# Kernel tuning notes

Measured on AMD Instinct MI355X. Metric: run time of the kernel, lower is better.

Reference implementation:

```python
import jax, jax.numpy as jnp
import numpy as np

B, T, C, H, W = 1, 8, 128, 64, 64
F = 64  # num_feat


def setup_inputs() -> dict:
    key = jax.random.key(0)
    ks = jax.random.split(key, 8)
    return {
        "input1": jax.random.normal(ks[0], (B, T, C, H, W), jnp.float32),
        "input2": jax.random.normal(ks[1], (B, T, C, H, W), jnp.float32),
        "W1": jax.random.normal(ks[2], (F, C), jnp.float32) * 0.05,
        "b1": jax.random.normal(ks[3], (F,), jnp.float32) * 0.05,
        "W2": jax.random.normal(ks[4], (F, C), jnp.float32) * 0.05,
        "b2": jax.random.normal(ks[5], (F,), jnp.float32) * 0.05,
        "W3": jax.random.normal(ks[6], (F, C), jnp.float32) * 0.05,
        "b3": jax.random.normal(ks[7], (F,), jnp.float32) * 0.05,
    }


def reference(input1, input2, W1, b1, W2, b2, W3, b3):
    # act == 0 (ReLU branch). Conv1d(kernel=1) == per-position linear projection.
    b, t, c, h, w = input1.shape
    n = h * w
    x1 = input1.reshape(b, t, c, n)  # matches transpose(1,2).reshape then frame slice
    x2 = input2.reshape(b, t, c, n)
    q = jnp.einsum('fc,btcn->btnf', W1, x1) + b1          # [B,T,N,F]
    k = jnp.einsum('fc,btcn->btnf', W2, x2) + b2          # [B,T,N,F]
    g = jnp.einsum('fc,btcn->btnf', W3, x1) + b3          # [B,T,N,F]
    scores = jax.nn.relu(jnp.einsum('btnf,btmf->btnm', q, k))  # [B,T,N,N]
    out = jnp.einsum('btnm,btmf->btnf', scores, g)        # [B,T,N,F]
    # view([B,H,W,F]).permute(0,3,1,2), stacked over T -> [B,T,F,H,W]
    return out.reshape(b, t, h, w, -1).transpose(0, 1, 4, 2, 3)
```

## Files before the change

kernel.cpp:

```cpp
#include <hip/hip_runtime.h>
#include <hip/hip_bf16.h>

constexpr int T = 8;
constexpr int C = 128;
constexpr int N = 4096;
constexpr int F = 64;

typedef __bf16 bf16x8 __attribute__((ext_vector_type(8)));
typedef __bf16 bf16x4 __attribute__((ext_vector_type(4)));
typedef float  f32x4  __attribute__((ext_vector_type(4)));

__global__ __launch_bounds__(256) void prep_w_kernel(
    const float* __restrict__ W1, const float* __restrict__ W2,
    const float* __restrict__ W3, __bf16* __restrict__ Wb)
{
    int i = blockIdx.x * 256 + threadIdx.x;
    const float* Ws[3] = {W1, W2, W3};
    int p = i >> 13, r = i & 8191;
    Wb[i] = (__bf16)Ws[p][r];
}

__global__ __launch_bounds__(256) void zero_out_kernel(float* __restrict__ out)
{
    int i = blockIdx.x * 256 + threadIdx.x;
    ((f32x4*)out)[i] = (f32x4){0.f, 0.f, 0.f, 0.f};
}

__global__ __launch_bounds__(256) void proj_kernel(
    const float* __restrict__ x1, const float* __restrict__ x2,
    const __bf16* __restrict__ Wb,
    const float* __restrict__ b1, const float* __restrict__ b2,
    const float* __restrict__ b3,
    __bf16* __restrict__ Qb, __bf16* __restrict__ Kb, __bf16* __restrict__ Gw)
{
    const int t  = blockIdx.x >> 6;
    const int nb = blockIdx.x & 63;
    const int n0 = nb * 64;

    constexpr int XS = C + 8;
    __shared__ __bf16 Xt1[64 * XS];
    __shared__ __bf16 Xt2[64 * XS];

    const int tid = threadIdx.x;
#pragma unroll
    for (int rep = 0; rep < 32; ++rep) {
        int idx = rep * 256 + tid;
        int c = idx >> 6, nl = idx & 63;
        size_t goff = ((size_t)t * C + c) * (size_t)N + n0 + nl;
        Xt1[nl * XS + c] = (__bf16)x1[goff];
        Xt2[nl * XS + c] = (__bf16)x2[goff];
    }
    __syncthreads();

    const int wave = tid >> 6, lane = tid & 63;
    const int quad = lane >> 4, l16 = lane & 15;

    bf16x8 a1[4], a2[4];
#pragma unroll
    for (int cc = 0; cc < 4; ++cc) {
        a1[cc] = *(const bf16x8*)&Xt1[(wave * 16 + l16) * XS + cc * 32 + quad * 8];
        a2[cc] = *(const bf16x8*)&Xt2[(wave * 16 + l16) * XS + cc * 32 + quad * 8];
    }

#pragma unroll
    for (int p = 0; p < 2; ++p) {
        const __bf16* W    = Wb + (size_t)p * F * C;
        const float*  bias = p ? b2 : b1;
        __bf16*       O    = p ? Kb : Qb;

        f32x4 acc[4];
#pragma unroll
        for (int ft = 0; ft < 4; ++ft) acc[ft] = (f32x4){0.f, 0.f, 0.f, 0.f};
#pragma unroll
        for (int cc = 0; cc < 4; ++cc) {
#pragma unroll
            for (int ft = 0; ft < 4; ++ft) {
                bf16x8 b = *(const bf16x8*)&W[(ft * 16 + l16) * C + cc * 32 + quad * 8];
                bf16x8 a = p ? a2[cc] : a1[cc];
                acc[ft] = __builtin_amdgcn_mfma_f32_16x16x32_bf16(a, b, acc[ft], 0, 0, 0);
            }
        }
#pragma unroll
        for (int ft = 0; ft < 4; ++ft) {
            int f = ft * 16 + l16;
            float bv = bias[f];
#pragma unroll
            for (int r = 0; r < 4; ++r) {
                int n = n0 + wave * 16 + quad * 4 + r;
                O[((size_t)t * N + n) * F + f] = (__bf16)(acc[ft][r] + bv);
            }
        }
    }

    {
        const __bf16* W3b = Wb + (size_t)2 * F * C;
        bf16x8 wa[4];
#pragma unroll
        for (int cc = 0; cc < 4; ++cc)
            wa[cc] = *(const bf16x8*)&W3b[(wave * 16 + l16) * C + cc * 32 + quad * 8];

        f32x4 acc[4];
#pragma unroll
        for (int nt = 0; nt < 4; ++nt) acc[nt] = (f32x4){0.f, 0.f, 0.f, 0.f};
#pragma unroll
        for (int cc = 0; cc < 4; ++cc) {
#pragma unroll
            for (int nt = 0; nt < 4; ++nt) {
                bf16x8 b = *(const bf16x8*)&Xt1[(nt * 16 + l16) * XS + cc * 32 + quad * 8];
                acc[nt] = __builtin_amdgcn_mfma_f32_16x16x32_bf16(wa[cc], b, acc[nt], 0, 0, 0);
            }
        }
#pragma unroll
        for (int nt = 0; nt < 4; ++nt) {
#pragma unroll
            for (int r = 0; r < 4; ++r) {
                int f = wave * 16 + quad * 4 + r;
                int n = n0 + nt * 16 + l16;
                Gw[((size_t)t * F + f) * (size_t)N + n] = (__bf16)(acc[nt][r] + b3[f]);
            }
        }
    }
}

constexpr int KSPLIT = 2;

__global__ __launch_bounds__(256) void attn_kernel(
    const __bf16* __restrict__ Qb, const __bf16* __restrict__ Kb,
    const __bf16* __restrict__ Gw, float* __restrict__ out)
{
    const int ks = blockIdx.x & (KSPLIT - 1);
    const int qb = (blockIdx.x / KSPLIT) & 31;
    const int t  = blockIdx.x / (KSPLIT * 32);
    const int q0 = qb * 128;

    constexpr int KS = 72;
    __shared__ __bf16 Kt[64 * KS];
    __shared__ __bf16 Gt[64 * KS];
    __shared__ __bf16 Sb[128 * KS];

    const int tid = threadIdx.x, wave = tid >> 6, lane = tid & 63;
    const int quad = lane >> 4, l16 = lane & 15;

    bf16x8 qf[2][2];
#pragma unroll
    for (int qg = 0; qg < 2; ++qg) {
        const __bf16* qrow = &Qb[((size_t)t * N + q0 + wave * 32 + qg * 16 + l16) * F];
        qf[qg][0] = *(const bf16x8*)&qrow[quad * 8];
        qf[qg][1] = *(const bf16x8*)&qrow[32 + quad * 8];
    }

    f32x4 oacc[4][2];
#pragma unroll
    for (int ft = 0; ft < 4; ++ft)
#pragma unroll
        for (int qg = 0; qg < 2; ++qg) oacc[ft][qg] = (f32x4){0.f, 0.f, 0.f, 0.f};

    const int kb_lo = ks * (N / 64 / KSPLIT);
    const int kb_hi = kb_lo + (N / 64 / KSPLIT);

    const int r8a = tid >> 3,          c8a = (tid & 7) * 8;
    const int r8b = (tid + 256) >> 3,  c8b = c8a;

    bf16x8 kv0, kv1, gv0, gv1;
    {
        const int k0 = kb_lo * 64;
        kv0 = *(const bf16x8*)&Kb[((size_t)t * N + k0 + r8a) * F + c8a];
        kv1 = *(const bf16x8*)&Kb[((size_t)t * N + k0 + r8b) * F + c8b];
        gv0 = *(const bf16x8*)&Gw[((size_t)t * F + r8a) * (size_t)N + k0 + c8a];
        gv1 = *(const bf16x8*)&Gw[((size_t)t * F + r8b) * (size_t)N + k0 + c8b];
    }

    for (int kb = kb_lo; kb < kb_hi; ++kb) {
        __syncthreads();
        *(bf16x8*)&Kt[r8a * KS + c8a] = kv0;
        *(bf16x8*)&Kt[r8b * KS + c8b] = kv1;
        *(bf16x8*)&Gt[r8a * KS + c8a] = gv0;
        *(bf16x8*)&Gt[r8b * KS + c8b] = gv1;
        __syncthreads();

        if (kb + 1 < kb_hi) {
            const int k0 = (kb + 1) * 64;
            kv0 = *(const bf16x8*)&Kb[((size_t)t * N + k0 + r8a) * F + c8a];
            kv1 = *(const bf16x8*)&Kb[((size_t)t * N + k0 + r8b) * F + c8b];
            gv0 = *(const bf16x8*)&Gw[((size_t)t * F + r8a) * (size_t)N + k0 + c8a];
            gv1 = *(const bf16x8*)&Gw[((size_t)t * F + r8b) * (size_t)N + k0 + c8b];
        }

#pragma unroll
        for (int nt = 0; nt < 4; ++nt) {
            bf16x8 k0f = *(const bf16x8*)&Kt[(nt * 16 + l16) * KS + quad * 8];
            bf16x8 k1f = *(const bf16x8*)&Kt[(nt * 16 + l16) * KS + 32 + quad * 8];
#pragma unroll
            for (int qg = 0; qg < 2; ++qg) {
                f32x4 s = (f32x4){0.f, 0.f, 0.f, 0.f};
                s = __builtin_amdgcn_mfma_f32_16x16x32_bf16(k0f, qf[qg][0], s, 0, 0, 0);
                s = __builtin_amdgcn_mfma_f32_16x16x32_bf16(k1f, qf[qg][1], s, 0, 0, 0);
                bf16x4 sp;
#pragma unroll
                for (int r = 0; r < 4; ++r) sp[r] = (__bf16)fmaxf(s[r], 0.f);
                *(bf16x4*)&Sb[(wave * 32 + qg * 16 + l16) * KS + nt * 16 + quad * 4] = sp;
            }
        }

        bf16x8 sf[2][2];
#pragma unroll
        for (int qg = 0; qg < 2; ++qg) {
            const __bf16* srow = &Sb[(wave * 32 + qg * 16 + l16) * KS];
            sf[qg][0] = *(const bf16x8*)&srow[quad * 8];
            sf[qg][1] = *(const bf16x8*)&srow[32 + quad * 8];
        }
#pragma unroll
        for (int ft = 0; ft < 4; ++ft) {
            bf16x8 g0 = *(const bf16x8*)&Gt[(ft * 16 + l16) * KS + quad * 8];
            bf16x8 g1 = *(const bf16x8*)&Gt[(ft * 16 + l16) * KS + 32 + quad * 8];
#pragma unroll
            for (int qg = 0; qg < 2; ++qg) {
                oacc[ft][qg] = __builtin_amdgcn_mfma_f32_16x16x32_bf16(g0, sf[qg][0], oacc[ft][qg], 0, 0, 0);
                oacc[ft][qg] = __builtin_amdgcn_mfma_f32_16x16x32_bf16(g1, sf[qg][1], oacc[ft][qg], 0, 0, 0);
            }
        }
    }

#pragma unroll
    for (int ft = 0; ft < 4; ++ft)
#pragma unroll
        for (int qg = 0; qg < 2; ++qg)
#pragma unroll
            for (int r = 0; r < 4; ++r) {
                int f = ft * 16 + quad * 4 + r;
                int q = q0 + wave * 32 + qg * 16 + l16;
                unsafeAtomicAdd(&out[((size_t)t * F + f) * (size_t)N + q], oacc[ft][qg][r]);
            }
}

extern "C" void kernel_launch(void* const* d_in, const int* in_sizes, int n_in,
                              void* d_out, int out_size, void* d_ws, size_t ws_size,
                              hipStream_t stream) {
    const float* x1 = (const float*)d_in[0];
    const float* x2 = (const float*)d_in[1];
    const float* W1 = (const float*)d_in[2];
    const float* b1 = (const float*)d_in[3];
    const float* W2 = (const float*)d_in[4];
    const float* b2 = (const float*)d_in[5];
    const float* W3 = (const float*)d_in[6];
    const float* b3 = (const float*)d_in[7];
    float* out = (float*)d_out;

    __bf16* Qb = (__bf16*)d_ws;
    __bf16* Kb = Qb + (size_t)T * N * F;
    __bf16* Gw = Kb + (size_t)T * N * F;
    __bf16* Wb = Gw + (size_t)T * N * F;

    prep_w_kernel<<<dim3(3 * F * C / 256), dim3(256), 0, stream>>>(W1, W2, W3, Wb);
    proj_kernel<<<dim3(T * (N / 64)), dim3(256), 0, stream>>>(
        x1, x2, Wb, b1, b2, b3, Qb, Kb, Gw);
    zero_out_kernel<<<dim3(T * F * N / 4 / 256), dim3(256), 0, stream>>>(out);
    attn_kernel<<<dim3(T * 32 * KSPLIT), dim3(256), 0, stream>>>(Qb, Kb, Gw, out);
}
```

Baseline: 162.3 us.

## Fuse weight prep and output zeroing into projection, enlarge attention query tile

Removes the separate weight-conversion and output-zeroing kernels. The projection kernel now zeroes its slice of the output, converts fp32 weights to bf16 on the fly, and loads x directly into MFMA fragments without an LDS transpose. The attention kernel now processes 256 queries per block (64 per wave) with KSPLIT raised to 4, which doubles K/G reuse per LDS tile while keeping the same grid size. The trade is higher register and LDS pressure, uncoalesced strided x loads, and redundant weight conversion in every block.

Measured after the change: 166.7 us. 1.03x slower.

```diff
diff --git a/kernel.cpp b/kernel.cpp
--- a/kernel.cpp
+++ b/kernel.cpp
@@ -10,150 +10,109 @@
 typedef __bf16 bf16x4 __attribute__((ext_vector_type(4)));
 typedef float  f32x4  __attribute__((ext_vector_type(4)));
 
-__global__ __launch_bounds__(256) void prep_w_kernel(
-    const float* __restrict__ W1, const float* __restrict__ W2,
-    const float* __restrict__ W3, __bf16* __restrict__ Wb)
-{
-    int i = blockIdx.x * 256 + threadIdx.x;
-    const float* Ws[3] = {W1, W2, W3};
-    int p = i >> 13, r = i & 8191;
-    Wb[i] = (__bf16)Ws[p][r];
-}
-
-__global__ __launch_bounds__(256) void zero_out_kernel(float* __restrict__ out)
-{
-    int i = blockIdx.x * 256 + threadIdx.x;
-    ((f32x4*)out)[i] = (f32x4){0.f, 0.f, 0.f, 0.f};
-}
-
 __global__ __launch_bounds__(256) void proj_kernel(
     const float* __restrict__ x1, const float* __restrict__ x2,
-    const __bf16* __restrict__ Wb,
-    const float* __restrict__ b1, const float* __restrict__ b2,
-    const float* __restrict__ b3,
-    __bf16* __restrict__ Qb, __bf16* __restrict__ Kb, __bf16* __restrict__ Gw)
+    const float* __restrict__ W1, const float* __restrict__ b1,
+    const float* __restrict__ W2, const float* __restrict__ b2,
+    const float* __restrict__ W3, const float* __restrict__ b3,
+    __bf16* __restrict__ Qb, __bf16* __restrict__ Kb, __bf16* __restrict__ Gw,
+    float* __restrict__ out)
 {
-    const int t  = blockIdx.x >> 6;
-    const int nb = blockIdx.x & 63;
-    const int n0 = nb * 64;
-
-    constexpr int XS = C + 8;
-    __shared__ __bf16 Xt1[64 * XS];
-    __shared__ __bf16 Xt2[64 * XS];
-
-    const int tid = threadIdx.x;
-#pragma unroll
-    for (int rep = 0; rep < 32; ++rep) {
-        int idx = rep * 256 + tid;
-        int c = idx >> 6, nl = idx & 63;
-        size_t goff = ((size_t)t * C + c) * (size_t)N + n0 + nl;
-        Xt1[nl * XS + c] = (__bf16)x1[goff];
-        Xt2[nl * XS + c] = (__bf16)x2[goff];
-    }
-    __syncthreads();
-
-    const int wave = tid >> 6, lane = tid & 63;
+    const int t   = blockIdx.x >> 6;
+    const int nb  = blockIdx.x & 63;
+    const int tid = threadIdx.x, wave = tid >> 6, lane = tid & 63;
     const int quad = lane >> 4, l16 = lane & 15;
-
-    bf16x8 a1[4], a2[4];
+    const int nw = nb * 64 + wave * 16;
+
+    {
+        f32x4* o4 = (f32x4*)out + (size_t)blockIdx.x * 1024;
+#pragma unroll
+        for (int i = 0; i < 4; ++i) o4[i * 256 + tid] = (f32x4){0.f, 0.f, 0.f, 0.f};
+    }
+
+    bf16x8 xf1[4], xf2[4];
 #pragma unroll
     for (int cc = 0; cc < 4; ++cc) {
-        a1[cc] = *(const bf16x8*)&Xt1[(wave * 16 + l16) * XS + cc * 32 + quad * 8];
-        a2[cc] = *(const bf16x8*)&Xt2[(wave * 16 + l16) * XS + cc * 32 + quad * 8];
-    }
-
-#pragma unroll
-    for (int p = 0; p < 2; ++p) {
-        const __bf16* W    = Wb + (size_t)p * F * C;
-        const float*  bias = p ? b2 : b1;
-        __bf16*       O    = p ? Kb : Qb;
-
-        f32x4 acc[4];
-#pragma unroll
-        for (int ft = 0; ft < 4; ++ft) acc[ft] = (f32x4){0.f, 0.f, 0.f, 0.f};
-#pragma unroll
-        for (int cc = 0; cc < 4; ++cc) {
-#pragma unroll
-            for (int ft = 0; ft < 4; ++ft) {
-                bf16x8 b = *(const bf16x8*)&W[(ft * 16 + l16) * C + cc * 32 + quad * 8];
-                bf16x8 a = p ? a2[cc] : a1[cc];
-                acc[ft] = __builtin_amdgcn_mfma_f32_16x16x32_bf16(a, b, acc[ft], 0, 0, 0);
-            }
-        }
-#pragma unroll
-        for (int ft = 0; ft < 4; ++ft) {
-            int f = ft * 16 + l16;
-            float bv = bias[f];
-#pragma unroll
-            for (int r = 0; r < 4; ++r) {
-                int n = n0 + wave * 16 + quad * 4 + r;
-                O[((size_t)t * N + n) * F + f] = (__bf16)(acc[ft][r] + bv);
-            }
-        }
-    }
-
-    {
-        const __bf16* W3b = Wb + (size_t)2 * F * C;
-        bf16x8 wa[4];
-#pragma unroll
-        for (int cc = 0; cc < 4; ++cc)
-            wa[cc] = *(const bf16x8*)&W3b[(wave * 16 + l16) * C + cc * 32 + quad * 8];
-
-        f32x4 acc[4];
-#pragma unroll
-        for (int nt = 0; nt < 4; ++nt) acc[nt] = (f32x4){0.f, 0.f, 0.f, 0.f};
-#pragma unroll
-        for (int cc = 0; cc < 4; ++cc) {
-#pragma unroll
-            for (int nt = 0; nt < 4; ++nt) {
-                bf16x8 b = *(const bf16x8*)&Xt1[(nt * 16 + l16) * XS + cc * 32 + quad * 8];
-                acc[nt] = __builtin_amdgcn_mfma_f32_16x16x32_bf16(wa[cc], b, acc[nt], 0, 0, 0);
-            }
-        }
-#pragma unroll
-        for (int nt = 0; nt < 4; ++nt) {
-#pragma unroll
-            for (int r = 0; r < 4; ++r) {
-                int f = wave * 16 + quad * 4 + r;
-                int n = n0 + nt * 16 + l16;
-                Gw[((size_t)t * F + f) * (size_t)N + n] = (__bf16)(acc[nt][r] + b3[f]);
+#pragma unroll
+        for (int j = 0; j < 8; ++j) {
+            size_t off = ((size_t)t * C + cc * 32 + quad * 8 + j) * (size_t)N + nw + l16;
+            xf1[cc][j] = (__bf16)x1[off];
+            xf2[cc][j] = (__bf16)x2[off];
+        }
+    }
+
+    const float* Ws[3] = {W1, W2, W3};
+    const float* bs[3] = {b1, b2, b3};
+
+#pragma unroll
+    for (int p = 0; p < 3; ++p) {
+        const float* W    = Ws[p];
+        const float* bias = bs[p];
+#pragma unroll
+        for (int fb = 0; fb < 4; ++fb) {
+            f32x4 acc = (f32x4){0.f, 0.f, 0.f, 0.f};
+#pragma unroll
+            for (int cc = 0; cc < 4; ++cc) {
+                const f32x4* wp = (const f32x4*)&W[(fb * 16 + l16) * C + cc * 32 + quad * 8];
+                f32x4 w0 = wp[0], w1 = wp[1];
+                bf16x8 wf;
+                wf[0] = (__bf16)w0[0]; wf[1] = (__bf16)w0[1];
+                wf[2] = (__bf16)w0[2]; wf[3] = (__bf16)w0[3];
+                wf[4] = (__bf16)w1[0]; wf[5] = (__bf16)w1[1];
+                wf[6] = (__bf16)w1[2]; wf[7] = (__bf16)w1[3];
+                bf16x8 xb = (p == 1) ? xf2[cc] : xf1[cc];
+                acc = __builtin_amdgcn_mfma_f32_16x16x32_bf16(wf, xb, acc, 0, 0, 0);
+            }
+            if (p < 2) {
+                __bf16* O = p ? Kb : Qb;
+                bf16x4 ov;
+#pragma unroll
+                for (int r = 0; r < 4; ++r)
+                    ov[r] = (__bf16)(acc[r] + bias[fb * 16 + quad * 4 + r]);
+                *(bf16x4*)&O[((size_t)t * N + nw + l16) * F + fb * 16 + quad * 4] = ov;
+            } else {
+#pragma unroll
+                for (int r = 0; r < 4; ++r) {
+                    int f = fb * 16 + quad * 4 + r;
+                    Gw[((size_t)t * F + f) * (size_t)N + nw + l16] = (__bf16)(acc[r] + bias[f]);
+                }
             }
         }
     }
 }
 
-constexpr int KSPLIT = 2;
+constexpr int KSPLIT = 4;
 
 __global__ __launch_bounds__(256) void attn_kernel(
     const __bf16* __restrict__ Qb, const __bf16* __restrict__ Kb,
     const __bf16* __restrict__ Gw, float* __restrict__ out)
 {
     const int ks = blockIdx.x & (KSPLIT - 1);
-    const int qb = (blockIdx.x / KSPLIT) & 31;
-    const int t  = blockIdx.x / (KSPLIT * 32);
-    const int q0 = qb * 128;
+    const int qb = (blockIdx.x / KSPLIT) & 15;
+    const int t  = blockIdx.x >> 6;
+    const int q0 = qb * 256;
 
     constexpr int KS = 72;
     __shared__ __bf16 Kt[64 * KS];
     __shared__ __bf16 Gt[64 * KS];
-    __shared__ __bf16 Sb[128 * KS];
+    __shared__ __bf16 Sb[256 * KS];
 
     const int tid = threadIdx.x, wave = tid >> 6, lane = tid & 63;
     const int quad = lane >> 4, l16 = lane & 15;
 
-    bf16x8 qf[2][2];
-#pragma unroll
-    for (int qg = 0; qg < 2; ++qg) {
-        const __bf16* qrow = &Qb[((size_t)t * N + q0 + wave * 32 + qg * 16 + l16) * F];
+    bf16x8 qf[4][2];
+#pragma unroll
+    for (int qg = 0; qg < 4; ++qg) {
+        const __bf16* qrow = &Qb[((size_t)t * N + q0 + wave * 64 + qg * 16 + l16) * F];
         qf[qg][0] = *(const bf16x8*)&qrow[quad * 8];
         qf[qg][1] = *(const bf16x8*)&qrow[32 + quad * 8];
     }
 
-    f32x4 oacc[4][2];
+    f32x4 oacc[4][4];
 #pragma unroll
     for (int ft = 0; ft < 4; ++ft)
 #pragma unroll
-        for (int qg = 0; qg < 2; ++qg) oacc[ft][qg] = (f32x4){0.f, 0.f, 0.f, 0.f};
+        for (int qg = 0; qg < 4; ++qg) oacc[ft][qg] = (f32x4){0.f, 0.f, 0.f, 0.f};
 
     const int kb_lo = ks * (N / 64 / KSPLIT);
     const int kb_hi = kb_lo + (N / 64 / KSPLIT);
@@ -191,21 +150,21 @@
             bf16x8 k0f = *(const bf16x8*)&Kt[(nt * 16 + l16) * KS + quad * 8];
             bf16x8 k1f = *(const bf16x8*)&Kt[(nt * 16 + l16) * KS + 32 + quad * 8];
 #pragma unroll
-            for (int qg = 0; qg < 2; ++qg) {
+            for (int qg = 0; qg < 4; ++qg) {
                 f32x4 s = (f32x4){0.f, 0.f, 0.f, 0.f};
                 s = __builtin_amdgcn_mfma_f32_16x16x32_bf16(k0f, qf[qg][0], s, 0, 0, 0);
                 s = __builtin_amdgcn_mfma_f32_16x16x32_bf16(k1f, qf[qg][1], s, 0, 0, 0);
                 bf16x4 sp;
 #pragma unroll
                 for (int r = 0; r < 4; ++r) sp[r] = (__bf16)fmaxf(s[r], 0.f);
-                *(bf16x4*)&Sb[(wave * 32 + qg * 16 + l16) * KS + nt * 16 + quad * 4] = sp;
-            }
-        }
-
-        bf16x8 sf[2][2];
-#pragma unroll
-        for (int qg = 0; qg < 2; ++qg) {
-            const __bf16* srow = &Sb[(wave * 32 + qg * 16 + l16) * KS];
+                *(bf16x4*)&Sb[(wave * 64 + qg * 16 + l16) * KS + nt * 16 + quad * 4] = sp;
+            }
+        }
+
+        bf16x8 sf[4][2];
+#pragma unroll
+        for (int qg = 0; qg < 4; ++qg) {
+            const __bf16* srow = &Sb[(wave * 64 + qg * 16 + l16) * KS];
             sf[qg][0] = *(const bf16x8*)&srow[quad * 8];
             sf[qg][1] = *(const bf16x8*)&srow[32 + quad * 8];
         }
@@ -214,7 +173,7 @@
             bf16x8 g0 = *(const bf16x8*)&Gt[(ft * 16 + l16) * KS + quad * 8];
             bf16x8 g1 = *(const bf16x8*)&Gt[(ft * 16 + l16) * KS + 32 + quad * 8];
 #pragma unroll
-            for (int qg = 0; qg < 2; ++qg) {
+            for (int qg = 0; qg < 4; ++qg) {
                 oacc[ft][qg] = __builtin_amdgcn_mfma_f32_16x16x32_bf16(g0, sf[qg][0], oacc[ft][qg], 0, 0, 0);
                 oacc[ft][qg] = __builtin_amdgcn_mfma_f32_16x16x32_bf16(g1, sf[qg][1], oacc[ft][qg], 0, 0, 0);
             }
@@ -224,11 +183,11 @@
 #pragma unroll
     for (int ft = 0; ft < 4; ++ft)
 #pragma unroll
-        for (int qg = 0; qg < 2; ++qg)
+        for (int qg = 0; qg < 4; ++qg)
 #pragma unroll
             for (int r = 0; r < 4; ++r) {
                 int f = ft * 16 + quad * 4 + r;
-                int q = q0 + wave * 32 + qg * 16 + l16;
+                int q = q0 + wave * 64 + qg * 16 + l16;
                 unsafeAtomicAdd(&out[((size_t)t * F + f) * (size_t)N + q], oacc[ft][qg][r]);
             }
 }
@@ -249,11 +208,8 @@
     __bf16* Qb = (__bf16*)d_ws;
     __bf16* Kb = Qb + (size_t)T * N * F;
     __bf16* Gw = Kb + (size_t)T * N * F;
-    __bf16* Wb = Gw + (size_t)T * N * F;
-
-    prep_w_kernel<<<dim3(3 * F * C / 256), dim3(256), 0, stream>>>(W1, W2, W3, Wb);
+
     proj_kernel<<<dim3(T * (N / 64)), dim3(256), 0, stream>>>(
-        x1, x2, Wb, b1, b2, b3, Qb, Kb, Gw);
-    zero_out_kernel<<<dim3(T * F * N / 4 / 256), dim3(256), 0, stream>>>(out);
-    attn_kernel<<<dim3(T * 32 * KSPLIT), dim3(256), 0, stream>>>(Qb, Kb, Gw, out);
+        x1, x2, W1, b1, W2, b2, W3, b3, Qb, Kb, Gw, out);
+    attn_kernel<<<dim3(T * 16 * KSPLIT), dim3(256), 0, stream>>>(Qb, Kb, Gw, out);
 }
```
